# Kernel tuning notes

Measured on AMD Instinct MI355X. Metric: run time of the kernel, lower is better.

The kernel has to match this reference:

```python
import jax, jax.numpy as jnp
import numpy as np

B, L1, CTX_TXT, C, NH, HD = 2, 4096, 512, 2048, 16, 128
IMG_LEN = 257           # hard-coded image-context length in WanI2VCrossAttentionProcessor
L2 = IMG_LEN + CTX_TXT
EPS = 1e-6


def setup_inputs() -> dict:
    key = jax.random.key(0)
    ks = jax.random.split(key, 16)
    s = 0.02
    w = lambda k: jax.random.normal(k, (C, C), jnp.float32) * s
    bvec = lambda k: jax.random.normal(k, (C,), jnp.float32) * s
    return {
        "x": jax.random.normal(ks[0], (B, L1, C), jnp.float32),
        "context": jax.random.normal(ks[1], (B, L2, C), jnp.float32),
        "context_lens": jax.random.randint(ks[2], (B,), 1, CTX_TXT + 1, jnp.int32),
        "Wq": w(ks[3]), "bq": bvec(ks[4]), "gq": jnp.ones((C,), jnp.float32),
        "Wk": w(ks[5]), "bk": bvec(ks[6]), "gk": jnp.ones((C,), jnp.float32),
        "Wv": w(ks[7]), "bv": bvec(ks[8]),
        "Wki": w(ks[9]), "bki": bvec(ks[10]), "gki": jnp.ones((C,), jnp.float32),
        "Wvi": w(ks[11]), "bvi": bvec(ks[12]),
        "Wo": w(ks[13]), "bo": bvec(ks[14]),
    }


def rms_norm(x, g):
    # RMSNorm over full channel dim (applied before head reshape, as in source)
    return x * jax.lax.rsqrt(jnp.mean(x * x, axis=-1, keepdims=True) + EPS) * g


def attention(q, k, v, key_mask=None):
    # q: [b, Lq, n, d]; k, v: [b, Lk, n, d]
    scale = 1.0 / np.sqrt(HD).astype(np.float32)
    scores = jnp.einsum('bqnd,bknd->bnqk', q, k) * scale
    if key_mask is not None:
        scores = jnp.where(key_mask, scores, jnp.finfo(scores.dtype).min)
    probs = jax.nn.softmax(scores, axis=-1)
    return jnp.einsum('bnqk,bknd->bqnd', probs, v)


def reference(x, context, context_lens, Wq, bq, gq, Wk, bk, gk, Wv, bv,
              Wki, bki, gki, Wvi, bvi, Wo, bo):
    b = x.shape[0]
    ctx_img = context[:, :IMG_LEN]
    ctx_txt = context[:, IMG_LEN:]

    q = rms_norm(x @ Wq + bq, gq).reshape(b, -1, NH, HD)
    k = rms_norm(ctx_txt @ Wk + bk, gk).reshape(b, -1, NH, HD)
    v = (ctx_txt @ Wv + bv).reshape(b, -1, NH, HD)
    k_img = rms_norm(ctx_img @ Wki + bki, gki).reshape(b, -1, NH, HD)
    v_img = (ctx_img @ Wvi + bvi).reshape(b, -1, NH, HD)

    img_x = attention(q, k_img, v_img)  # no k_lens on image branch
    key_mask = (jnp.arange(CTX_TXT)[None, :] < context_lens[:, None])[:, None, None, :]
    txt_x = attention(q, k, v, key_mask)

    out = (txt_x + img_x).reshape(b, -1, NH * HD)
    return out @ Wo + bo
```

## Files before the change

### kernel.cpp

```cpp
#include <hip/hip_runtime.h>

typedef unsigned short u16;
typedef short short8 __attribute__((ext_vector_type(8)));
typedef float f32x4 __attribute__((ext_vector_type(4)));
typedef unsigned short u16x4 __attribute__((ext_vector_type(4)));

__device__ __forceinline__ u16 f2bf(float f) {
  unsigned u = __builtin_bit_cast(unsigned, f);
  u += 0x7fffu + ((u >> 16) & 1u);
  return (u16)(u >> 16);
}
__device__ __forceinline__ float bf2f(u16 s) {
  unsigned u = ((unsigned)s) << 16;
  return __builtin_bit_cast(float, u);
}
__device__ __forceinline__ unsigned cvtpk_bf16(float a, float b) {
  unsigned r;
  asm("v_cvt_pk_bf16_f32 %0, %1, %2" : "=v"(r) : "v"(a), "v"(b));
  return r;
}

#if __has_builtin(__builtin_amdgcn_exp2f)
#define EXP2F(x) __builtin_amdgcn_exp2f(x)
#else
#define EXP2F(x) exp2f(x)
#endif

#define MFMA32(a, b, c) __builtin_amdgcn_mfma_f32_16x16x32_bf16(a, b, c, 0, 0, 0)

#define GLDS16(gp, lp)                                                         \
  __builtin_amdgcn_global_load_lds(                                            \
      (__attribute__((address_space(1))) void*)(gp),                           \
      (__attribute__((address_space(3))) void*)(lp), 16, 0, 0)

__global__ __launch_bounds__(256) void cast_bf16_k(const float* __restrict__ in,
                                                   u16* __restrict__ out, int n4) {
  int i = blockIdx.x * 256 + threadIdx.x;
  if (i >= n4) return;
  float4 v = ((const float4*)in)[i];
  u16x4 o = { f2bf(v.x), f2bf(v.y), f2bf(v.z), f2bf(v.w) };
  ((u16x4*)out)[i] = o;
}

__global__ __launch_bounds__(256) void transw_k(const float* W0, const float* W1,
                                                const float* W2, const float* W3,
                                                const float* W4, const float* W5,
                                                u16* __restrict__ Wt) {
  int z = blockIdx.z;
  const float* W = z == 0 ? W0 : z == 1 ? W1 : z == 2 ? W2 : z == 3 ? W3 : z == 4 ? W4 : W5;
  u16* T = Wt + (size_t)z * 2048 * 2048;
  __shared__ float tile[64][65];
  int k0 = blockIdx.x * 64, n0 = blockIdx.y * 64;
  int c4 = (threadIdx.x & 15) * 4;
  int r = threadIdx.x >> 4;
#pragma unroll
  for (int i = 0; i < 4; ++i) {
    int row = r + i * 16;
    float4 v = *(const float4*)(W + (size_t)(k0 + row) * 2048 + n0 + c4);
    tile[row][c4 + 0] = v.x; tile[row][c4 + 1] = v.y;
    tile[row][c4 + 2] = v.z; tile[row][c4 + 3] = v.w;
  }
  __syncthreads();
#pragma unroll
  for (int i = 0; i < 4; ++i) {
    int nrow = r + i * 16;
    u16x4 o = { f2bf(tile[c4 + 0][nrow]), f2bf(tile[c4 + 1][nrow]),
                f2bf(tile[c4 + 2][nrow]), f2bf(tile[c4 + 3][nrow]) };
    *(u16x4*)(T + (size_t)(n0 + nrow) * 2048 + k0 + c4) = o;
  }
}

struct GemmJob {
  const u16* A; const u16* Bt; const float* bias; void* out;
  int M; int mode; int ldo;
};
struct GemmJobs { GemmJob j[8]; };

__global__ __launch_bounds__(256) void gemm_k(GemmJobs jobs) {
  GemmJob J = jobs.j[blockIdx.z];
  const int m0 = blockIdx.x * 128;
  if (m0 >= J.M) return;
  const int n0 = blockIdx.y * 128;
  __shared__ u16 Asm[128 * 32];
  __shared__ u16 Bsm[128 * 32];
  const int tid = threadIdx.x;
  const int lane = tid & 63;
  const int l15 = lane & 15, quad = lane >> 4;
  const int wave = tid >> 6;
  const int wr = (wave >> 1) * 64, wc = (wave & 1) * 64;
  f32x4 acc[4][4] = {};
  const int g0 = tid, g1 = tid + 256;
  const u16* ag0 = J.A + (size_t)(m0 + (g0 >> 2)) * 2048 + (g0 & 3) * 8;
  const u16* ag1 = J.A + (size_t)(m0 + (g1 >> 2)) * 2048 + (g1 & 3) * 8;
  const u16* bg0 = J.Bt + (size_t)(n0 + (g0 >> 2)) * 2048 + (g0 & 3) * 8;
  const u16* bg1 = J.Bt + (size_t)(n0 + (g1 >> 2)) * 2048 + (g1 & 3) * 8;
  u16* al0 = Asm + g0 * 8; u16* al1 = Asm + g1 * 8;
  u16* bl0 = Bsm + g0 * 8; u16* bl1 = Bsm + g1 * 8;
  for (int k0 = 0; k0 < 2048; k0 += 32) {
    GLDS16(ag0 + k0, al0);
    GLDS16(ag1 + k0, al1);
    GLDS16(bg0 + k0, bl0);
    GLDS16(bg1 + k0, bl1);
    __syncthreads();
    short8 af[4], bf[4];
#pragma unroll
    for (int mi = 0; mi < 4; ++mi)
      af[mi] = *(const short8*)(Asm + (wr + mi * 16 + l15) * 32 + quad * 8);
#pragma unroll
    for (int ni = 0; ni < 4; ++ni)
      bf[ni] = *(const short8*)(Bsm + (wc + ni * 16 + l15) * 32 + quad * 8);
#pragma unroll
    for (int mi = 0; mi < 4; ++mi)
#pragma unroll
      for (int ni = 0; ni < 4; ++ni)
        acc[mi][ni] = __builtin_amdgcn_mfma_f32_16x16x32_bf16(af[mi], bf[ni], acc[mi][ni], 0, 0, 0);
    __syncthreads();
  }
#pragma unroll
  for (int mi = 0; mi < 4; ++mi) {
#pragma unroll
    for (int ni = 0; ni < 4; ++ni) {
      int nn = n0 + wc + ni * 16 + l15;
      float bv = J.bias[nn];
#pragma unroll
      for (int r = 0; r < 4; ++r) {
        int mm = m0 + wr + mi * 16 + quad * 4 + r;
        if (mm >= J.M) continue;
        float v = acc[mi][ni][r] + bv;
        if (J.mode == 0) {
          ((u16*)J.out)[(size_t)mm * J.ldo + nn] = f2bf(v);
        } else if (J.mode == 1) {
          int ml = mm & 31;
          int mp = (mm & ~31) | (((ml >> 2) & 3) * 8 + (ml >> 4) * 4 + (ml & 3));
          ((u16*)J.out)[(size_t)nn * J.ldo + mp] = f2bf(v);
        } else {
          ((float*)J.out)[(size_t)mm * J.ldo + nn] = v;
        }
      }
    }
  }
}

__global__ __launch_bounds__(512, 2) void gemm256_k(const u16* __restrict__ A,
                                                    const u16* __restrict__ Bt,
                                                    const float* __restrict__ bias,
                                                    void* __restrict__ out,
                                                    int mode) {
  const int m0 = blockIdx.x * 256, n0 = blockIdx.y * 256;
  __shared__ u16 lds[2][2][256 * 32];
  const int tid = threadIdx.x, lane = tid & 63;
  const int l15 = lane & 15, quad = lane >> 4;
  const int wave = tid >> 6;
  const int wr = wave >> 2;
  const int wc = wave & 3;
  const int srow = tid >> 2;
  const int sc = ((tid & 3) ^ ((srow >> 1) & 3)) * 8;
  const u16* Ag = A + (size_t)(m0 + srow) * 2048 + sc;
  const u16* Bg = Bt + (size_t)(n0 + srow) * 2048 + sc;
  const int lxor = (l15 >> 1) & 3;
  f32x4 acc[8][4] = {};

  auto stage = [&](int buf, int kt) {
    const size_t ko = (size_t)kt * 32;
    u16* dA = &lds[buf][0][tid * 8];
    u16* dB = &lds[buf][1][tid * 8];
    GLDS16(Ag + ko, dA);
    GLDS16(Ag + (size_t)128 * 2048 + ko, dA + 4096);
    GLDS16(Bg + ko, dB);
    GLDS16(Bg + (size_t)128 * 2048 + ko, dB + 4096);
  };

  stage(0, 0);
  for (int t = 0; t < 64; ++t) {
    const int cb = t & 1;
    __syncthreads();
    if (t + 1 < 64) stage(cb ^ 1, t + 1);
    const u16* Ab = &lds[cb][0][(size_t)wr * 128 * 32];
    const u16* Bb = &lds[cb][1][0];
    short8 bfr[4];
#pragma unroll
    for (int ni = 0; ni < 4; ++ni) {
      const int rn = wc * 64 + ni * 16 + l15;
      bfr[ni] = *(const short8*)(Bb + rn * 32 + ((quad ^ lxor) * 8));
    }
#pragma unroll
    for (int mi = 0; mi < 8; ++mi) {
      const int rm = mi * 16 + l15;
      short8 a = *(const short8*)(Ab + rm * 32 + ((quad ^ lxor) * 8));
      __builtin_amdgcn_s_setprio(1);
#pragma unroll
      for (int ni = 0; ni < 4; ++ni)
        acc[mi][ni] = MFMA32(a, bfr[ni], acc[mi][ni]);
      __builtin_amdgcn_s_setprio(0);
    }
  }
#pragma unroll
  for (int mi = 0; mi < 8; ++mi) {
#pragma unroll
    for (int ni = 0; ni < 4; ++ni) {
      const int nn = n0 + wc * 64 + ni * 16 + l15;
      const float bv = bias[nn];
      const int mm = m0 + wr * 128 + mi * 16 + quad * 4;
      if (mode == 0) {
        u16* op = (u16*)out + (size_t)mm * 2048 + nn;
#pragma unroll
        for (int r = 0; r < 4; ++r) op[(size_t)r * 2048] = f2bf(acc[mi][ni][r] + bv);
      } else {
        float* op = (float*)out + (size_t)mm * 2048 + nn;
#pragma unroll
        for (int r = 0; r < 4; ++r) op[(size_t)r * 2048] = acc[mi][ni][r] + bv;
      }
    }
  }
}

__global__ __launch_bounds__(256) void rmsnorm_k(u16* __restrict__ buf,
                                                 const float* __restrict__ g) {
  const int row = blockIdx.x, tid = threadIdx.x;
  u16* p = buf + (size_t)row * 2048 + tid * 8;
  short8 v = *(short8*)p;
  float x[8]; float s = 0.f;
#pragma unroll
  for (int i = 0; i < 8; ++i) { x[i] = bf2f((u16)v[i]); s += x[i] * x[i]; }
#pragma unroll
  for (int o = 1; o < 64; o <<= 1) s += __shfl_xor(s, o, 64);
  __shared__ float ws4[4];
  if ((tid & 63) == 0) ws4[tid >> 6] = s;
  __syncthreads();
  float tot = ws4[0] + ws4[1] + ws4[2] + ws4[3];
  float scale = rsqrtf(tot * (1.0f / 2048.0f) + 1e-6f);
  const float* gp = g + tid * 8;
  short8 o8;
#pragma unroll
  for (int i = 0; i < 8; ++i) o8[i] = (short)f2bf(x[i] * scale * gp[i]);
  *(short8*)p = o8;
}

__global__ __launch_bounds__(512) void attn_k(const u16* __restrict__ Q,
                                              const u16* __restrict__ Kt,
                                              const u16* __restrict__ Vt,
                                              const u16* __restrict__ Ki,
                                              const u16* __restrict__ Vi,
                                              const int* __restrict__ lens,
                                              u16* __restrict__ out) {
  const int lid = blockIdx.x + 16 * (blockIdx.y + 16 * blockIdx.z);
  const int w = (lid & 7) * 64 + (lid >> 3);
  const int qx = w & 15, hb = w >> 4;
  const int h = hb & 15, b = hb >> 4;

  const int tid = threadIdx.x, lane = tid & 63, wave = tid >> 6;
  const int l15 = lane & 15, quad = lane >> 4;
  const int qbase = qx * 256 + wave * 32;
  const float scale2 = 0.12752358514837517f;
  const float NEGINF = -__builtin_inff();
  __shared__ u16 Ksm[2][2][32 * 128];
  __shared__ u16 Vsm[2][2][128 * 32];

  short8 qf[2][4];
#pragma unroll
  for (int h2 = 0; h2 < 2; ++h2) {
    const u16* qb = Q + ((size_t)(b * 4096 + qbase + h2 * 16 + l15)) * 2048 + h * 128 + quad * 8;
#pragma unroll
    for (int kc = 0; kc < 4; ++kc) qf[h2][kc] = *(const short8*)(qb + kc * 32);
  }

  const int krow = tid >> 4;
  const int kcc = ((tid & 15) ^ (krow & 7)) * 8;
  const int vd = tid >> 2;
  const int vcs = ((tid & 3) ^ ((vd >> 1) & 3)) * 8;
  const int kxor = l15 & 7;
  const int vxor = (l15 >> 1) & 3;

  f32x4 accv[2][8];
  u16x4 oimg[2][8];
  float run_m[2], run_l[2];

  auto phase = [&](const u16* Kb, const u16* Vb, int Lv, int LK) {
    run_m[0] = run_m[1] = NEGINF;
    run_l[0] = run_l[1] = 0.f;
#pragma unroll
    for (int h2 = 0; h2 < 2; ++h2)
#pragma unroll
      for (int dt = 0; dt < 8; ++dt)
#pragma unroll
        for (int r = 0; r < 4; ++r) accv[h2][dt][r] = 0.f;
    const u16* kg = Kb + (size_t)krow * 2048 + kcc;
    const u16* vg = Vb + (size_t)vd * LK + vcs;
    const int ntiles = (Lv + 63) >> 6;
    auto stage = [&](int buf, int t) {
      const int kvA = t * 64;
      const int sA = (kvA < LK - 32) ? kvA : (LK - 32);
      const int sB = (kvA + 32 < LK - 32) ? (kvA + 32) : (LK - 32);
      GLDS16(kg + (size_t)sA * 2048, &Ksm[buf][0][tid * 8]);
      GLDS16(kg + (size_t)sB * 2048, &Ksm[buf][1][tid * 8]);
      GLDS16(vg + sA, &Vsm[buf][0][tid * 8]);
      GLDS16(vg + sB, &Vsm[buf][1][tid * 8]);
    };
    stage(0, 0);
    __syncthreads();
    for (int t = 0; t < ntiles; ++t) {
      const int cb = t & 1;
      if (t + 1 < ntiles) stage(cb ^ 1, t + 1);

      f32x4 s[2][4];
#pragma unroll
      for (int h2 = 0; h2 < 2; ++h2)
#pragma unroll
        for (int kb = 0; kb < 4; ++kb)
#pragma unroll
          for (int r = 0; r < 4; ++r) s[h2][kb][r] = 0.f;
      {
        short8 kA[2][4];
#pragma unroll
        for (int kc = 0; kc < 4; ++kc) {
          const int c0 = ((kc * 4 + quad) ^ kxor) * 8;
          kA[0][kc] = *(const short8*)(&Ksm[cb][0][l15 * 128 + c0]);
          kA[1][kc] = *(const short8*)(&Ksm[cb][0][(16 + l15) * 128 + c0]);
        }
        __builtin_amdgcn_s_setprio(1);
#pragma unroll
        for (int h2 = 0; h2 < 2; ++h2)
#pragma unroll
          for (int kc = 0; kc < 4; ++kc) {
            s[h2][0] = MFMA32(kA[0][kc], qf[h2][kc], s[h2][0]);
            s[h2][1] = MFMA32(kA[1][kc], qf[h2][kc], s[h2][1]);
          }
        __builtin_amdgcn_s_setprio(0);
      }
      {
        short8 kB[2][4];
#pragma unroll
        for (int kc = 0; kc < 4; ++kc) {
          const int c0 = ((kc * 4 + quad) ^ kxor) * 8;
          kB[0][kc] = *(const short8*)(&Ksm[cb][1][l15 * 128 + c0]);
          kB[1][kc] = *(const short8*)(&Ksm[cb][1][(16 + l15) * 128 + c0]);
        }
        __builtin_amdgcn_s_setprio(1);
#pragma unroll
        for (int h2 = 0; h2 < 2; ++h2)
#pragma unroll
          for (int kc = 0; kc < 4; ++kc) {
            s[h2][2] = MFMA32(kB[0][kc], qf[h2][kc], s[h2][2]);
            s[h2][3] = MFMA32(kB[1][kc], qf[h2][kc], s[h2][3]);
          }
        __builtin_amdgcn_s_setprio(0);
      }

      const int kvA = t * 64;
      if (kvA + 64 > Lv) {
#pragma unroll
        for (int h2 = 0; h2 < 2; ++h2)
#pragma unroll
          for (int kb = 0; kb < 4; ++kb)
#pragma unroll
            for (int r = 0; r < 4; ++r) {
              const int ki = kvA + kb * 16 + quad * 4 + r;
              if (ki >= Lv) s[h2][kb][r] = NEGINF;
            }
      }

      float al[2];
      short8 pfA[2], pfB[2];
#pragma unroll
      for (int h2 = 0; h2 < 2; ++h2) {
        float m0 = fmaxf(fmaxf(s[h2][0][0], s[h2][0][1]), fmaxf(s[h2][0][2], s[h2][0][3]));
        float m1 = fmaxf(fmaxf(s[h2][1][0], s[h2][1][1]), fmaxf(s[h2][1][2], s[h2][1][3]));
        float m2 = fmaxf(fmaxf(s[h2][2][0], s[h2][2][1]), fmaxf(s[h2][2][2], s[h2][2][3]));
        float m3 = fmaxf(fmaxf(s[h2][3][0], s[h2][3][1]), fmaxf(s[h2][3][2], s[h2][3][3]));
        float mx = fmaxf(fmaxf(m0, m1), fmaxf(m2, m3));
        mx = fmaxf(mx, __shfl_xor(mx, 16, 64));
        mx = fmaxf(mx, __shfl_xor(mx, 32, 64));
        const float nm = fmaxf(run_m[h2], mx);
        al[h2] = EXP2F((run_m[h2] - nm) * scale2);
        run_m[h2] = nm;
        const float nmc = -nm * scale2;
        float p[4][4], psum = 0.f;
#pragma unroll
        for (int kb = 0; kb < 4; ++kb)
#pragma unroll
          for (int r = 0; r < 4; ++r) {
            p[kb][r] = EXP2F(__builtin_fmaf(s[h2][kb][r], scale2, nmc));
            psum += p[kb][r];
          }
        run_l[h2] = __builtin_fmaf(run_l[h2], al[h2], psum);
        union { short8 s8; unsigned u[4]; } pa, pb;
        pa.u[0] = cvtpk_bf16(p[0][0], p[0][1]);
        pa.u[1] = cvtpk_bf16(p[0][2], p[0][3]);
        pa.u[2] = cvtpk_bf16(p[1][0], p[1][1]);
        pa.u[3] = cvtpk_bf16(p[1][2], p[1][3]);
        pb.u[0] = cvtpk_bf16(p[2][0], p[2][1]);
        pb.u[1] = cvtpk_bf16(p[2][2], p[2][3]);
        pb.u[2] = cvtpk_bf16(p[3][0], p[3][1]);
        pb.u[3] = cvtpk_bf16(p[3][2], p[3][3]);
        pfA[h2] = pa.s8;
        pfB[h2] = pb.s8;
      }
      if (t != 0 && __ballot((al[0] < 1.0f) || (al[1] < 1.0f))) {
#pragma unroll
        for (int h2 = 0; h2 < 2; ++h2)
#pragma unroll
          for (int dt = 0; dt < 8; ++dt)
#pragma unroll
            for (int r = 0; r < 4; ++r) accv[h2][dt][r] *= al[h2];
      }

      __builtin_amdgcn_s_setprio(1);
#pragma unroll
      for (int dt = 0; dt < 8; ++dt) {
        const int vo = (dt * 16 + l15) * 32 + ((quad ^ vxor) * 8);
        short8 vfA = *(const short8*)(&Vsm[cb][0][vo]);
        short8 vfB = *(const short8*)(&Vsm[cb][1][vo]);
        accv[0][dt] = MFMA32(vfA, pfA[0], accv[0][dt]);
        accv[1][dt] = MFMA32(vfA, pfA[1], accv[1][dt]);
        accv[0][dt] = MFMA32(vfB, pfB[0], accv[0][dt]);
        accv[1][dt] = MFMA32(vfB, pfB[1], accv[1][dt]);
      }
      __builtin_amdgcn_s_setprio(0);
      __syncthreads();
    }
  };

  const u16* Kb_i = Ki + (size_t)(b * 288) * 2048 + h * 128;
  const u16* Vb_i = Vi + ((size_t)(b * 16 + h) * 128) * 288;
  phase(Kb_i, Vb_i, 257, 288);
#pragma unroll
  for (int h2 = 0; h2 < 2; ++h2) {
    float a = run_l[h2] + __shfl_xor(run_l[h2], 16, 64);
    float lt = a + __shfl_xor(a, 32, 64);
    float inv = 1.0f / lt;
#pragma unroll
    for (int dt = 0; dt < 8; ++dt) {
      u16x4 w2 = { f2bf(accv[h2][dt][0] * inv), f2bf(accv[h2][dt][1] * inv),
                   f2bf(accv[h2][dt][2] * inv), f2bf(accv[h2][dt][3] * inv) };
      oimg[h2][dt] = w2;
    }
  }
  const u16* Kb_t = Kt + (size_t)(b * 512) * 2048 + h * 128;
  const u16* Vb_t = Vt + ((size_t)(b * 16 + h) * 128) * 512;
  phase(Kb_t, Vb_t, lens[b], 512);
#pragma unroll
  for (int h2 = 0; h2 < 2; ++h2) {
    float a = run_l[h2] + __shfl_xor(run_l[h2], 16, 64);
    float lt = a + __shfl_xor(a, 32, 64);
    float inv = 1.0f / lt;
    u16* ob = out + ((size_t)(b * 4096 + qbase + h2 * 16 + l15)) * 2048 + h * 128 + quad * 4;
#pragma unroll
    for (int dt = 0; dt < 8; ++dt) {
      u16x4 w2 = { f2bf(bf2f(oimg[h2][dt][0]) + accv[h2][dt][0] * inv),
                   f2bf(bf2f(oimg[h2][dt][1]) + accv[h2][dt][1] * inv),
                   f2bf(bf2f(oimg[h2][dt][2]) + accv[h2][dt][2] * inv),
                   f2bf(bf2f(oimg[h2][dt][3]) + accv[h2][dt][3] * inv) };
      *(u16x4*)(ob + dt * 16) = w2;
    }
  }
}

extern "C" void kernel_launch(void* const* d_in, const int* in_sizes, int n_in,
                              void* d_out, int out_size, void* d_ws, size_t ws_size,
                              hipStream_t stream) {
  const float* x   = (const float*)d_in[0];
  const float* ctx = (const float*)d_in[1];
  const int* lens  = (const int*)d_in[2];
  const float* Wq  = (const float*)d_in[3];
  const float* bq  = (const float*)d_in[4];
  const float* gq  = (const float*)d_in[5];
  const float* Wk  = (const float*)d_in[6];
  const float* bk  = (const float*)d_in[7];
  const float* gk  = (const float*)d_in[8];
  const float* Wv  = (const float*)d_in[9];
  const float* bv  = (const float*)d_in[10];
  const float* Wki = (const float*)d_in[11];
  const float* bki = (const float*)d_in[12];
  const float* gki = (const float*)d_in[13];
  const float* Wvi = (const float*)d_in[14];
  const float* bvi = (const float*)d_in[15];
  const float* Wo  = (const float*)d_in[16];
  const float* bo  = (const float*)d_in[17];
  float* out = (float*)d_out;

  char* p = (char*)d_ws;
  u16* x_bf   = (u16*)p; p += (size_t)8192 * 2048 * 2;
  u16* ctx_bf = (u16*)p; p += (size_t)2 * 769 * 2048 * 2;
  u16* Wt     = (u16*)p; p += (size_t)6 * 2048 * 2048 * 2;
  u16* Qb     = (u16*)p; p += (size_t)8192 * 2048 * 2;
  u16* Ktxt   = (u16*)p; p += (size_t)2 * 512 * 2048 * 2;
  u16* Vtt    = (u16*)p; p += (size_t)2 * 16 * 128 * 512 * 2;
  u16* Kimg   = (u16*)p; p += (size_t)2 * 288 * 2048 * 2;
  u16* Vti    = (u16*)p; p += (size_t)2 * 16 * 128 * 288 * 2;
  u16* attn_o = x_bf;

  cast_bf16_k<<<16384, 256, 0, stream>>>(x, x_bf, 8192 * 2048 / 4);
  cast_bf16_k<<<3076, 256, 0, stream>>>(ctx, ctx_bf, 2 * 769 * 2048 / 4);
  transw_k<<<dim3(32, 32, 6), 256, 0, stream>>>(Wq, Wk, Wv, Wki, Wvi, Wo, Wt);

  gemm256_k<<<dim3(32, 8), 512, 0, stream>>>(x_bf, Wt + 0ull * 4194304, bq, Qb, 0);

  GemmJobs jc = {};
  for (int b = 0; b < 2; ++b) {
    const u16* txtA = ctx_bf + (size_t)(b * 769 + 257) * 2048;
    const u16* imgA = ctx_bf + (size_t)(b * 769) * 2048;
    jc.j[0 + b] = { txtA, Wt + 1ull * 4194304, bk,  Ktxt + (size_t)b * 512 * 2048, 512, 0, 2048 };
    jc.j[2 + b] = { txtA, Wt + 2ull * 4194304, bv,  Vtt  + (size_t)b * 2048 * 512, 512, 1, 512 };
    jc.j[4 + b] = { imgA, Wt + 3ull * 4194304, bki, Kimg + (size_t)b * 288 * 2048, 257, 0, 2048 };
    jc.j[6 + b] = { imgA, Wt + 4ull * 4194304, bvi, Vti  + (size_t)b * 2048 * 288, 257, 1, 288 };
  }
  gemm_k<<<dim3(4, 16, 8), 256, 0, stream>>>(jc);

  rmsnorm_k<<<8192, 256, 0, stream>>>(Qb, gq);
  rmsnorm_k<<<1024, 256, 0, stream>>>(Ktxt, gk);
  rmsnorm_k<<<576, 256, 0, stream>>>(Kimg, gki);

  attn_k<<<dim3(16, 16, 2), 512, 0, stream>>>(Qb, Ktxt, Vtt, Kimg, Vti, lens, attn_o);

  gemm256_k<<<dim3(32, 8), 512, 0, stream>>>(attn_o, Wt + 5ull * 4194304, bo, out, 1);
}
```

Measured before the change: 514.9 us.

## Double-buffer small GEMM, triple-buffer large GEMM, and lazily rescale softmax max

The 128-tile GEMM moves to double-buffered LDS with prefetch of the next k-slice and raised MFMA priority, dropping the second barrier per iteration. The 256-tile GEMM moves to a 3-stage LDS ring with explicit vmcnt waits and raw barriers, so two loads stay in flight. The attention softmax only raises the running max when the new max exceeds it by a threshold, skipping rescales. The extra LDS can lower occupancy, and the manual waitcnt/barrier scheme and the lazy max rely on exact ordering and numeric headroom for correctness.

```diff
diff --git a/kernel.cpp b/kernel.cpp
--- a/kernel.cpp
+++ b/kernel.cpp
@@ -81,8 +81,8 @@
   const int m0 = blockIdx.x * 128;
   if (m0 >= J.M) return;
   const int n0 = blockIdx.y * 128;
-  __shared__ u16 Asm[128 * 32];
-  __shared__ u16 Bsm[128 * 32];
+  __shared__ u16 Asm[2][128 * 32];
+  __shared__ u16 Bsm[2][128 * 32];
   const int tid = threadIdx.x;
   const int lane = tid & 63;
   const int l15 = lane & 15, quad = lane >> 4;
@@ -94,27 +94,32 @@
   const u16* ag1 = J.A + (size_t)(m0 + (g1 >> 2)) * 2048 + (g1 & 3) * 8;
   const u16* bg0 = J.Bt + (size_t)(n0 + (g0 >> 2)) * 2048 + (g0 & 3) * 8;
   const u16* bg1 = J.Bt + (size_t)(n0 + (g1 >> 2)) * 2048 + (g1 & 3) * 8;
-  u16* al0 = Asm + g0 * 8; u16* al1 = Asm + g1 * 8;
-  u16* bl0 = Bsm + g0 * 8; u16* bl1 = Bsm + g1 * 8;
+
+  auto stage = [&](int buf, int k0) {
+    GLDS16(ag0 + k0, &Asm[buf][g0 * 8]);
+    GLDS16(ag1 + k0, &Asm[buf][g1 * 8]);
+    GLDS16(bg0 + k0, &Bsm[buf][g0 * 8]);
+    GLDS16(bg1 + k0, &Bsm[buf][g1 * 8]);
+  };
+  stage(0, 0);
   for (int k0 = 0; k0 < 2048; k0 += 32) {
-    GLDS16(ag0 + k0, al0);
-    GLDS16(ag1 + k0, al1);
-    GLDS16(bg0 + k0, bl0);
-    GLDS16(bg1 + k0, bl1);
+    const int cb = (k0 >> 5) & 1;
     __syncthreads();
+    if (k0 + 32 < 2048) stage(cb ^ 1, k0 + 32);
     short8 af[4], bf[4];
 #pragma unroll
     for (int mi = 0; mi < 4; ++mi)
-      af[mi] = *(const short8*)(Asm + (wr + mi * 16 + l15) * 32 + quad * 8);
+      af[mi] = *(const short8*)(&Asm[cb][(wr + mi * 16 + l15) * 32 + quad * 8]);
 #pragma unroll
     for (int ni = 0; ni < 4; ++ni)
-      bf[ni] = *(const short8*)(Bsm + (wc + ni * 16 + l15) * 32 + quad * 8);
+      bf[ni] = *(const short8*)(&Bsm[cb][(wc + ni * 16 + l15) * 32 + quad * 8]);
+    __builtin_amdgcn_s_setprio(1);
 #pragma unroll
     for (int mi = 0; mi < 4; ++mi)
 #pragma unroll
       for (int ni = 0; ni < 4; ++ni)
         acc[mi][ni] = __builtin_amdgcn_mfma_f32_16x16x32_bf16(af[mi], bf[ni], acc[mi][ni], 0, 0, 0);
-    __syncthreads();
+    __builtin_amdgcn_s_setprio(0);
   }
 #pragma unroll
   for (int mi = 0; mi < 4; ++mi) {
@@ -147,7 +152,7 @@
                                                     void* __restrict__ out,
                                                     int mode) {
   const int m0 = blockIdx.x * 256, n0 = blockIdx.y * 256;
-  __shared__ u16 lds[2][2][256 * 32];
+  __shared__ u16 lds[3][2][256 * 32];
   const int tid = threadIdx.x, lane = tid & 63;
   const int l15 = lane & 15, quad = lane >> 4;
   const int wave = tid >> 6;
@@ -171,10 +176,13 @@
   };
 
   stage(0, 0);
+  stage(1, 1);
+  int cb = 0;
   for (int t = 0; t < 64; ++t) {
-    const int cb = t & 1;
-    __syncthreads();
-    if (t + 1 < 64) stage(cb ^ 1, t + 1);
+    if (t < 63) asm volatile("s_waitcnt vmcnt(4)" ::: "memory");
+    else        asm volatile("s_waitcnt vmcnt(0)" ::: "memory");
+    __builtin_amdgcn_s_barrier();
+    if (t + 2 < 64) stage((cb == 0) ? 2 : cb - 1, t + 2);
     const u16* Ab = &lds[cb][0][(size_t)wr * 128 * 32];
     const u16* Bb = &lds[cb][1][0];
     short8 bfr[4];
@@ -193,6 +201,7 @@
         acc[mi][ni] = MFMA32(a, bfr[ni], acc[mi][ni]);
       __builtin_amdgcn_s_setprio(0);
     }
+    cb = (cb == 2) ? 0 : cb + 1;
   }
 #pragma unroll
   for (int mi = 0; mi < 8; ++mi) {
@@ -370,7 +379,7 @@
         float mx = fmaxf(fmaxf(m0, m1), fmaxf(m2, m3));
         mx = fmaxf(mx, __shfl_xor(mx, 16, 64));
         mx = fmaxf(mx, __shfl_xor(mx, 32, 64));
-        const float nm = fmaxf(run_m[h2], mx);
+        const float nm = (mx - run_m[h2] > 62.0f) ? mx : run_m[h2];
         al[h2] = EXP2F((run_m[h2] - nm) * scale2);
         run_m[h2] = nm;
         const float nmc = -nm * scale2;
```

Result: no change. 514.2 us (-0.1%).
